# Performance work log

Hardware: AMD Instinct MI355X
Metric: run time of the kernel (lower is better)

The kernel has to match this reference:

```python
import jax, jax.numpy as jnp
import numpy as np

B, S, T, K = 128, 4, 16, 36   # questions, answer slots (hardcoded 4), max tags/slot, num boxes
VD, QD, H = 256, 256, 256
NB = B * S * T                # total tag rows = leading dim of v, q


def setup_inputs() -> dict:
    key = jax.random.key(0)
    ks = jax.random.split(key, 8)
    tags_attention = jnp.ones((B, S, T), dtype=jnp.int32)  # all slots full -> sum == NB
    v = jax.random.normal(ks[0], (NB, K, VD), jnp.float32)
    q = jax.random.normal(ks[1], (NB, QD), jnp.float32)
    # binary box mask, first box always valid
    bm = (jax.random.uniform(ks[2], (B, K)) < 0.85).astype(jnp.float32)
    box_mask = bm.at[:, 0].set(1.0)
    Wv = jax.random.normal(ks[3], (H, VD), jnp.float32) / np.sqrt(VD).astype(np.float32)
    bv = jnp.zeros((H,), jnp.float32)
    Wq = jax.random.normal(ks[4], (H, QD), jnp.float32) / np.sqrt(QD).astype(np.float32)
    bq = jnp.zeros((H,), jnp.float32)
    Wl = jax.random.normal(ks[5], (1, H), jnp.float32) / np.sqrt(H).astype(np.float32)
    bl = jnp.zeros((1,), jnp.float32)
    return dict(v=v, q=q, box_mask=box_mask, tags_attention=tags_attention,
                Wv=Wv, bv=bv, Wq=Wq, bq=bq, Wl=Wl, bl=bl)


def reference(v, q, box_mask, tags_attention, Wv, bv, Wq, bq, Wl, bl):
    # FCNet projections (weight-normed Linear + ReLU; dropout inactive at eval)
    v_proj = jax.nn.relu(jnp.einsum('nkd,hd->nkh', v, Wv) + bv)          # [N,K,H]
    q_proj = jax.nn.relu(q @ Wq.T + bq)                                   # [N,H]
    joint = v_proj * q_proj[:, None, :]                                   # [N,K,H]
    logits = jnp.einsum('nkh,h->nk', joint, Wl[0]) + bl[0]                # [N,K]

    # pad_sequence: ragged rows -> [B,S,T,K] via per-slot offsets + masked gather
    Bq, Ss, Tt = tags_attention.shape
    lengths = tags_attention.sum(-1)                                      # [B,S]
    flat_len = lengths.reshape(-1)
    offsets = jnp.concatenate([jnp.zeros((1,), flat_len.dtype),
                               jnp.cumsum(flat_len)[:-1]]).reshape(Bq, Ss)
    t = jnp.arange(Tt)
    idx = offsets[:, :, None] + t                                         # [B,S,T]
    valid = t[None, None, :] < lengths[:, :, None]                        # [B,S,T]
    gathered = logits[jnp.clip(idx, 0, logits.shape[0] - 1)]              # [B,S,T,K]
    logits_batch = jnp.where(valid[..., None], gathered, 0.0)

    # masked_softmax (r2c style): softmax(x*mask)*mask, renormalized
    mask = box_mask[:, None, None, :]                                     # [B,1,1,K]
    w = jax.nn.softmax(logits_batch * mask, axis=-1) * mask
    w = w / (w.sum(-1, keepdims=True) + 1e-13)
    return w
```

## Files before the change

### kernel.cpp

```cpp
#include <hip/hip_runtime.h>
#include <stdint.h>

#define NBROWS 8192
#define KBOX   36
#define MROWS  (NBROWS * KBOX)
#define HDIM   256

typedef __attribute__((ext_vector_type(8))) short bf16x8;
typedef __attribute__((ext_vector_type(4))) float f32x4;

__device__ __forceinline__ unsigned short f2bf(float f) {
  unsigned int u = __float_as_uint(f);
  return (unsigned short)((u + 0x7fffu + ((u >> 16) & 1u)) >> 16);
}

__global__ void cvt_kernel(const float* __restrict__ Wv, const float* __restrict__ Wq,
                           unsigned short* __restrict__ wvb, unsigned short* __restrict__ wqb) {
  int i = blockIdx.x * 256 + threadIdx.x;
  wvb[i] = f2bf(Wv[i]);
  wqb[i] = f2bf(Wq[i]);
}

template<int MODE>
__global__ __launch_bounds__(256, 4)
void gemm_kernel(const float* __restrict__ Amat,
                 const unsigned short* __restrict__ Wbf,
                 const float* __restrict__ bias,
                 const float* __restrict__ wl,
                 const float* __restrict__ g,
                 float* __restrict__ outp,
                 const float* __restrict__ blp)
{
  __shared__ unsigned short Asm[64 * 32];
  __shared__ unsigned short Bsm[256 * 32];
  __shared__ float bias_sm[256];
  __shared__ float aux_sm[4 * 256];
  __shared__ float partial[64 * 4];

  const int t    = threadIdx.x;
  const int lane = t & 63;
  const int wid  = t >> 6;
  const int r0   = blockIdx.x * 64;

  bias_sm[t] = bias[t];
  int n_base = 0;
  if (MODE == 0) {
    aux_sm[t] = wl[t];
  } else {
    n_base = r0 / KBOX;
    #pragma unroll
    for (int i = 0; i < 4; ++i) {
      int idx = t + i * 256;
      int n = n_base + (idx >> 8);
      if (n > NBROWS - 1) n = NBROWS - 1;
      aux_sm[idx] = g[(size_t)n * 256 + (idx & 255)];
    }
  }

  f32x4 acc[4][4];
  #pragma unroll
  for (int a = 0; a < 4; ++a)
    #pragma unroll
    for (int b = 0; b < 4; ++b) acc[a][b] = (f32x4)0.f;

  const int arow = t >> 2;
  const int ako  = t & 3;
  const float* asrc = Amat + (size_t)(r0 + arow) * 256 + ako * 8;
  unsigned short* adst = &Asm[arow * 32 + (ako ^ ((arow >> 1) & 3)) * 8];

  for (int kk = 0; kk < 8; ++kk) {
    const int d0 = kk * 32;
    __syncthreads();
    {
      const float4* s4 = (const float4*)(asrc + d0);
      float4 v0 = s4[0];
      float4 v1 = s4[1];
      uint4 pk;
      pk.x = (unsigned)f2bf(v0.x) | ((unsigned)f2bf(v0.y) << 16);
      pk.y = (unsigned)f2bf(v0.z) | ((unsigned)f2bf(v0.w) << 16);
      pk.z = (unsigned)f2bf(v1.x) | ((unsigned)f2bf(v1.y) << 16);
      pk.w = (unsigned)f2bf(v1.z) | ((unsigned)f2bf(v1.w) << 16);
      *(uint4*)adst = pk;
    }
    #pragma unroll
    for (int i = 0; i < 4; ++i) {
      int u = t + i * 256;
      int brow = u >> 2, bko = u & 3;
      uint4 val = *(const uint4*)&Wbf[brow * 256 + d0 + bko * 8];
      *(uint4*)&Bsm[brow * 32 + (bko ^ ((brow >> 1) & 3)) * 8] = val;
    }
    __syncthreads();
    bf16x8 af[4], bfr[4];
    #pragma unroll
    for (int mf = 0; mf < 4; ++mf) {
      int row  = mf * 16 + (lane & 15);
      int phys = (lane >> 4) ^ ((row >> 1) & 3);
      af[mf] = *(const bf16x8*)&Asm[row * 32 + phys * 8];
    }
    #pragma unroll
    for (int nf = 0; nf < 4; ++nf) {
      int col  = wid * 64 + nf * 16 + (lane & 15);
      int phys = (lane >> 4) ^ ((col >> 1) & 3);
      bfr[nf] = *(const bf16x8*)&Bsm[col * 32 + phys * 8];
    }
    #pragma unroll
    for (int mf = 0; mf < 4; ++mf)
      #pragma unroll
      for (int nf = 0; nf < 4; ++nf)
        acc[mf][nf] = __builtin_amdgcn_mfma_f32_16x16x32_bf16(af[mf], bfr[nf], acc[mf][nf], 0, 0, 0);
  }

  if (MODE == 0) {
    #pragma unroll
    for (int mf = 0; mf < 4; ++mf)
      #pragma unroll
      for (int nf = 0; nf < 4; ++nf) {
        int col = wid * 64 + nf * 16 + (lane & 15);
        float bb = bias_sm[col];
        float ww = aux_sm[col];
        #pragma unroll
        for (int j = 0; j < 4; ++j) {
          int row = mf * 16 + ((lane >> 4) << 2) + j;
          float x = fmaxf(acc[mf][nf][j] + bb, 0.f) * ww;
          outp[(size_t)(r0 + row) * 256 + col] = x;
        }
      }
  } else {
    float s[4][4];
    #pragma unroll
    for (int mf = 0; mf < 4; ++mf) {
      #pragma unroll
      for (int j = 0; j < 4; ++j) {
        int row  = mf * 16 + ((lane >> 4) << 2) + j;
        int nloc = (r0 + row) / KBOX - n_base;
        const float* grow = &aux_sm[nloc * 256];
        float acc_s = 0.f;
        #pragma unroll
        for (int nf = 0; nf < 4; ++nf) {
          int col = wid * 64 + nf * 16 + (lane & 15);
          float x = acc[mf][nf][j] + bias_sm[col];
          acc_s += fmaxf(x, 0.f) * grow[col];
        }
        s[mf][j] = acc_s;
      }
    }
    #pragma unroll
    for (int mf = 0; mf < 4; ++mf)
      #pragma unroll
      for (int j = 0; j < 4; ++j) {
        float vv = s[mf][j];
        vv += __shfl_xor(vv, 1);
        vv += __shfl_xor(vv, 2);
        vv += __shfl_xor(vv, 4);
        vv += __shfl_xor(vv, 8);
        s[mf][j] = vv;
      }
    if ((lane & 15) == 0) {
      #pragma unroll
      for (int mf = 0; mf < 4; ++mf)
        #pragma unroll
        for (int j = 0; j < 4; ++j) {
          int row = mf * 16 + ((lane >> 4) << 2) + j;
          partial[row * 4 + wid] = s[mf][j];
        }
    }
    __syncthreads();
    if (t < 64) {
      float vv = partial[t * 4 + 0] + partial[t * 4 + 1] + partial[t * 4 + 2] + partial[t * 4 + 3];
      outp[r0 + t] = vv + blp[0];
    }
  }
}

__global__ __launch_bounds__(256)
void softmax_kernel(const float* __restrict__ logits, const float* __restrict__ box_mask,
                    float* __restrict__ outp) {
  int n = blockIdx.x * 4 + (threadIdx.x >> 6);
  int k = threadIdx.x & 63;
  int b = n >> 6;
  float l = 0.f, m = 0.f;
  if (k < KBOX) {
    m = box_mask[b * KBOX + k];
    l = logits[(size_t)n * KBOX + k];
  }
  bool act = (k < KBOX) && (m > 0.5f);
  float lm = act ? l : -3.0e38f;
  #pragma unroll
  for (int off = 32; off >= 1; off >>= 1) lm = fmaxf(lm, __shfl_xor(lm, off));
  float e = act ? expf(l - lm) : 0.f;
  float ssum = e;
  #pragma unroll
  for (int off = 32; off >= 1; off >>= 1) ssum += __shfl_xor(ssum, off);
  if (k < KBOX) outp[(size_t)n * KBOX + k] = e / ssum;
}

extern "C" void kernel_launch(void* const* d_in, const int* in_sizes, int n_in,
                              void* d_out, int out_size, void* d_ws, size_t ws_size,
                              hipStream_t stream) {
  const float* v        = (const float*)d_in[0];
  const float* q        = (const float*)d_in[1];
  const float* box_mask = (const float*)d_in[2];
  const float* Wv = (const float*)d_in[4];
  const float* bv = (const float*)d_in[5];
  const float* Wq = (const float*)d_in[6];
  const float* bq = (const float*)d_in[7];
  const float* Wl = (const float*)d_in[8];
  const float* bl = (const float*)d_in[9];
  float* outp = (float*)d_out;

  char* ws = (char*)d_ws;
  unsigned short* wvb = (unsigned short*)ws;
  unsigned short* wqb = (unsigned short*)(ws + 131072);
  float* g      = (float*)(ws + 262144);
  float* logits = (float*)(ws + 262144 + 8388608);

  cvt_kernel<<<256, 256, 0, stream>>>(Wv, Wq, wvb, wqb);
  gemm_kernel<0><<<NBROWS / 64, 256, 0, stream>>>(q, wqb, bq, Wl, nullptr, g, nullptr);
  gemm_kernel<1><<<MROWS / 64, 256, 0, stream>>>(v, wvb, bv, nullptr, g, logits, bl);
  softmax_kernel<<<NBROWS / 4, 256, 0, stream>>>(logits, box_mask, outp);
}
```

Before: 131.9 us.

## Software-pipeline GEMM loads with async global-to-LDS B tiles and A register ring

Rewrites the GEMM K-loop as a fully unrolled multi-stage pipeline. Weight tiles are copied straight into four LDS buffers with global_load_lds. Activation tiles are prefetched four steps ahead into a register ring, then converted into a double-buffered A LDS tile. This replaces two __syncthreads per iteration with one lgkmcnt wait plus barrier, and lowers launch_bounds occupancy to 2 to make room for the larger LDS and register footprint. The aim is to hide global memory latency on the large fp32 v stream. The cost is lower occupancy and reliance on vmcnt ordering for correctness of the async LDS loads.

```diff
diff --git a/kernel.cpp b/kernel.cpp
--- a/kernel.cpp
+++ b/kernel.cpp
@@ -1,10 +1,10 @@
 #include <hip/hip_runtime.h>
+#include <hip/hip_bf16.h>
 #include <stdint.h>
 
 #define NBROWS 8192
 #define KBOX   36
 #define MROWS  (NBROWS * KBOX)
-#define HDIM   256
 
 typedef __attribute__((ext_vector_type(8))) short bf16x8;
 typedef __attribute__((ext_vector_type(4))) float f32x4;
@@ -13,6 +13,26 @@
   unsigned int u = __float_as_uint(f);
   return (unsigned short)((u + 0x7fffu + ((u >> 16) & 1u)) >> 16);
 }
+
+__device__ __forceinline__ unsigned int pk2(float x, float y) {
+  __hip_bfloat16 hx = __float2bfloat16(x);
+  __hip_bfloat16 hy = __float2bfloat16(y);
+  unsigned short ux, uy;
+  __builtin_memcpy(&ux, &hx, 2);
+  __builtin_memcpy(&uy, &hy, 2);
+  return (unsigned)ux | ((unsigned)uy << 16);
+}
+
+__device__ __forceinline__ void gll16(const void* g, void* l) {
+  __builtin_amdgcn_global_load_lds((const __attribute__((address_space(1))) unsigned int*)g,
+                                   (__attribute__((address_space(3))) unsigned int*)l,
+                                   16, 0, 0);
+}
+
+#define LGKM_BARRIER() do {                                   \
+    asm volatile("s_waitcnt lgkmcnt(0)" ::: "memory");        \
+    asm volatile("s_barrier" ::: "memory");                   \
+  } while (0)
 
 __global__ void cvt_kernel(const float* __restrict__ Wv, const float* __restrict__ Wq,
                            unsigned short* __restrict__ wvb, unsigned short* __restrict__ wqb) {
@@ -22,7 +42,7 @@
 }
 
 template<int MODE>
-__global__ __launch_bounds__(256, 4)
+__global__ __launch_bounds__(256, 2)
 void gemm_kernel(const float* __restrict__ Amat,
                  const unsigned short* __restrict__ Wbf,
                  const float* __restrict__ bias,
@@ -31,8 +51,8 @@
                  float* __restrict__ outp,
                  const float* __restrict__ blp)
 {
-  __shared__ unsigned short Asm[64 * 32];
-  __shared__ unsigned short Bsm[256 * 32];
+  __shared__ unsigned short Asm[2][64 * 32];
+  __shared__ unsigned short Bsm[4][256 * 32];
   __shared__ float bias_sm[256];
   __shared__ float aux_sm[4 * 256];
   __shared__ float partial[64 * 4];
@@ -57,58 +77,93 @@
     }
   }
 
-  f32x4 acc[4][4];
-  #pragma unroll
-  for (int a = 0; a < 4; ++a)
-    #pragma unroll
-    for (int b = 0; b < 4; ++b) acc[a][b] = (f32x4)0.f;
+  int bh[4], bco[4];
+  #pragma unroll
+  for (int i = 0; i < 4; ++i) {
+    int h = wid * 64 + i * 16 + (lane >> 2);
+    bh[i]  = h;
+    bco[i] = ((lane & 3) ^ ((h >> 1) & 3)) * 8;
+  }
 
   const int arow = t >> 2;
   const int ako  = t & 3;
   const float* asrc = Amat + (size_t)(r0 + arow) * 256 + ako * 8;
-  unsigned short* adst = &Asm[arow * 32 + (ako ^ ((arow >> 1) & 3)) * 8];
-
-  for (int kk = 0; kk < 8; ++kk) {
-    const int d0 = kk * 32;
-    __syncthreads();
-    {
-      const float4* s4 = (const float4*)(asrc + d0);
-      float4 v0 = s4[0];
-      float4 v1 = s4[1];
-      uint4 pk;
-      pk.x = (unsigned)f2bf(v0.x) | ((unsigned)f2bf(v0.y) << 16);
-      pk.y = (unsigned)f2bf(v0.z) | ((unsigned)f2bf(v0.w) << 16);
-      pk.z = (unsigned)f2bf(v1.x) | ((unsigned)f2bf(v1.y) << 16);
-      pk.w = (unsigned)f2bf(v1.z) | ((unsigned)f2bf(v1.w) << 16);
-      *(uint4*)adst = pk;
-    }
-    #pragma unroll
-    for (int i = 0; i < 4; ++i) {
-      int u = t + i * 256;
-      int brow = u >> 2, bko = u & 3;
-      uint4 val = *(const uint4*)&Wbf[brow * 256 + d0 + bko * 8];
-      *(uint4*)&Bsm[brow * 32 + (bko ^ ((brow >> 1) & 3)) * 8] = val;
-    }
-    __syncthreads();
-    bf16x8 af[4], bfr[4];
-    #pragma unroll
-    for (int mf = 0; mf < 4; ++mf) {
-      int row  = mf * 16 + (lane & 15);
-      int phys = (lane >> 4) ^ ((row >> 1) & 3);
-      af[mf] = *(const bf16x8*)&Asm[row * 32 + phys * 8];
-    }
-    #pragma unroll
-    for (int nf = 0; nf < 4; ++nf) {
-      int col  = wid * 64 + nf * 16 + (lane & 15);
-      int phys = (lane >> 4) ^ ((col >> 1) & 3);
-      bfr[nf] = *(const bf16x8*)&Bsm[col * 32 + phys * 8];
-    }
-    #pragma unroll
-    for (int mf = 0; mf < 4; ++mf)
-      #pragma unroll
-      for (int nf = 0; nf < 4; ++nf)
-        acc[mf][nf] = __builtin_amdgcn_mfma_f32_16x16x32_bf16(af[mf], bfr[nf], acc[mf][nf], 0, 0, 0);
-  }
+  const int adst_off = arow * 32 + (ako ^ ((arow >> 1) & 3)) * 8;
+
+  f32x4 acc[4][4];
+  #pragma unroll
+  for (int a = 0; a < 4; ++a)
+    #pragma unroll
+    for (int b = 0; b < 4; ++b) acc[a][b] = (f32x4)0.f;
+
+  float4 ring[4][2];
+
+  #define GLLB(j) do {                                                            \
+      _Pragma("unroll")                                                           \
+      for (int i = 0; i < 4; ++i)                                                 \
+        gll16(Wbf + (size_t)bh[i] * 256 + (j) * 32 + bco[i],                      \
+              &Bsm[(j) & 3][(wid * 64 + i * 16) * 32]);                           \
+    } while (0)
+  #define AISS(j) do {                                                            \
+      ring[(j) & 3][0] = ((const float4*)(asrc + (j) * 32))[0];                   \
+      ring[(j) & 3][1] = ((const float4*)(asrc + (j) * 32))[1];                   \
+    } while (0)
+  #define ACVT(j) do {                                                            \
+      const float4 a0 = ring[(j) & 3][0];                                         \
+      const float4 a1 = ring[(j) & 3][1];                                         \
+      uint4 pk;                                                                   \
+      pk.x = pk2(a0.x, a0.y);                                                     \
+      pk.y = pk2(a0.z, a0.w);                                                     \
+      pk.z = pk2(a1.x, a1.y);                                                     \
+      pk.w = pk2(a1.z, a1.w);                                                     \
+      *(uint4*)&Asm[(j) & 1][adst_off] = pk;                                      \
+    } while (0)
+
+  GLLB(0); __builtin_amdgcn_sched_barrier(0); AISS(0); __builtin_amdgcn_sched_barrier(0);
+  GLLB(1); __builtin_amdgcn_sched_barrier(0); AISS(1); __builtin_amdgcn_sched_barrier(0);
+  GLLB(2); __builtin_amdgcn_sched_barrier(0); AISS(2); __builtin_amdgcn_sched_barrier(0);
+  GLLB(3); __builtin_amdgcn_sched_barrier(0); AISS(3); __builtin_amdgcn_sched_barrier(0);
+  ACVT(0);
+  LGKM_BARRIER();
+
+  #define STEP(kk) do {                                                           \
+    bf16x8 af[4], bfr[4];                                                         \
+    _Pragma("unroll")                                                             \
+    for (int mf = 0; mf < 4; ++mf) {                                              \
+      int row  = mf * 16 + (lane & 15);                                           \
+      int phys = (lane >> 4) ^ ((row >> 1) & 3);                                  \
+      af[mf] = *(const bf16x8*)&Asm[(kk) & 1][row * 32 + phys * 8];               \
+    }                                                                             \
+    _Pragma("unroll")                                                             \
+    for (int nf = 0; nf < 4; ++nf) {                                              \
+      int col  = wid * 64 + nf * 16 + (lane & 15);                                \
+      int phys = (lane >> 4) ^ ((col >> 1) & 3);                                  \
+      bfr[nf] = *(const bf16x8*)&Bsm[(kk) & 3][col * 32 + phys * 8];              \
+    }                                                                             \
+    _Pragma("unroll")                                                             \
+    for (int mf = 0; mf < 4; ++mf)                                                \
+      _Pragma("unroll")                                                           \
+      for (int nf = 0; nf < 4; ++nf)                                              \
+        acc[mf][nf] = __builtin_amdgcn_mfma_f32_16x16x32_bf16(af[mf], bfr[nf], acc[mf][nf], 0, 0, 0); \
+    if ((kk) <= 3) {     \
+      GLLB((kk) + 4);                                                             \
+      __builtin_amdgcn_sched_barrier(0);                                          \
+      AISS((kk) + 4);                                                             \
+      __builtin_amdgcn_sched_barrier(0);                                          \
+    }                                                                             \
+    if ((kk) <= 6) {                                                              \
+      ACVT((kk) + 1);   \
+      LGKM_BARRIER();                                                             \
+    }                                                                             \
+  } while (0)
+
+  STEP(0); STEP(1); STEP(2); STEP(3);
+  STEP(4); STEP(5); STEP(6); STEP(7);
+
+  #undef STEP
+  #undef GLLB
+  #undef AISS
+  #undef ACVT
 
   if (MODE == 0) {
     #pragma unroll
```

After: 140.9 us. 1.07x slower.
